# Kernel tuning notes

Hardware: AMD Instinct MI355X
Metric: run time of the kernel (lower is better)

The kernel has to match this reference:

```python
import jax, jax.numpy as jnp
import numpy as np

EMB = 1024
HEADS = 16
HEAD_DIM = EMB // HEADS
B, S = 4, 2048


def setup_inputs() -> dict:
    key = jax.random.key(0)
    ks = jax.random.split(key, 7)
    sc = 1.0 / np.sqrt(EMB)
    return {
        "query": jax.random.normal(ks[0], (B, S, EMB), jnp.float32),
        "key": jax.random.normal(ks[1], (B, S, EMB), jnp.float32),
        "value": jax.random.normal(ks[2], (B, S, EMB), jnp.float32),
        "Wq": jax.random.normal(ks[3], (EMB, EMB), jnp.float32) * sc,
        "Wk": jax.random.normal(ks[4], (EMB, EMB), jnp.float32) * sc,
        "Wv": jax.random.normal(ks[5], (EMB, EMB), jnp.float32) * sc,
        "Wo": jax.random.normal(ks[6], (EMB, EMB), jnp.float32) * sc,
    }


def reference(query, key, value, Wq, Wk, Wv, Wo):
    # nn.Linear applies x @ W^T; W stored as [out, in]
    def split_heads(x):  # [B,S,E] -> [B,H,S,D]
        return x.reshape(B, -1, HEADS, HEAD_DIM).transpose(0, 2, 1, 3)

    q = split_heads(query @ Wq.T)
    k = split_heads(key @ Wk.T)
    v = split_heads(value @ Wv.T)
    scores = jnp.einsum('bhse,bhte->bhst', q, k) / np.sqrt(HEAD_DIM).astype(np.float32)
    attn = jax.nn.softmax(scores, axis=-1)
    ctx = jnp.einsum('bhst,bhtd->bshd', attn, v)  # [B,S,H,D]
    out = ctx.reshape(B, -1, EMB) @ Wo.T
    return out
```

## Files before the change

kernel.cpp:

```cpp
#include <hip/hip_runtime.h>
#include <hip/hip_bf16.h>

#define EMB   1024
#define HEADS 16
#define HDIM  64
#define BB    4
#define SS    2048
#define MROWS (BB*SS)

typedef __bf16 bf16_t;
typedef __bf16 bf16x4_t __attribute__((ext_vector_type(4)));
typedef __bf16 bf16x8   __attribute__((ext_vector_type(8)));
typedef float  f32x4    __attribute__((ext_vector_type(4)));

__device__ __forceinline__ void glds16(const void* g, void* l) {
  __builtin_amdgcn_global_load_lds(
      (const __attribute__((address_space(1))) void*)g,
      (__attribute__((address_space(3))) void*)l, 16, 0, 0);
}

__launch_bounds__(256)
__global__ void cast_multi(const float* s0, const float* s1, const float* s2,
                           const float* s3, const float* s4, const float* s5,
                           const float* s6,
                           bf16_t* d0, bf16_t* d1, bf16_t* d2, bf16_t* d3,
                           bf16_t* d4, bf16_t* d5, bf16_t* d6, int nact) {
  const int z = blockIdx.z;
  if (z >= nact && blockIdx.x >= 512) return;
  const float* ss[7] = {s0, s1, s2, s3, s4, s5, s6};
  bf16_t*      dd[7] = {d0, d1, d2, d3, d4, d5, d6};
  const float* s = ss[z];
  bf16_t*      d = dd[z];
  const int i = (blockIdx.x*256 + threadIdx.x) * 8;
  const f32x4 a = *(const f32x4*)&s[i];
  const f32x4 b = *(const f32x4*)&s[i+4];
  bf16x8 r;
  r[0]=(bf16_t)a[0]; r[1]=(bf16_t)a[1]; r[2]=(bf16_t)a[2]; r[3]=(bf16_t)a[3];
  r[4]=(bf16_t)b[0]; r[5]=(bf16_t)b[1]; r[6]=(bf16_t)b[2]; r[7]=(bf16_t)b[3];
  *(bf16x8*)&d[i] = r;
}

__launch_bounds__(256)
__global__ void cast_f32_bf16(const float* __restrict__ src, bf16_t* __restrict__ dst) {
  const int i = (blockIdx.x*256 + threadIdx.x) * 8;
  const f32x4 a = *(const f32x4*)&src[i];
  const f32x4 b = *(const f32x4*)&src[i+4];
  bf16x8 r;
  r[0]=(bf16_t)a[0]; r[1]=(bf16_t)a[1]; r[2]=(bf16_t)a[2]; r[3]=(bf16_t)a[3];
  r[4]=(bf16_t)b[0]; r[5]=(bf16_t)b[1]; r[6]=(bf16_t)b[2]; r[7]=(bf16_t)b[3];
  *(bf16x8*)&dst[i] = r;
}

__device__ __forceinline__ void gemm_core(const bf16_t* __restrict__ A,
                                          const bf16_t* __restrict__ W,
                                          bf16_t* As, bf16_t* Bs,
                                          f32x4 acc[4][4],
                                          int bm0, int bn0,
                                          int wave, int lane) {
  const int quad = lane >> 4, l16 = lane & 15;
  const int wm = wave >> 1, wn = wave & 1;
  for (int k0 = 0; k0 < EMB; k0 += 32) {
#pragma unroll
    for (int j = 0; j < 2; ++j) {
      const int i   = wave*2 + j;
      const int row = i*16 + (lane >> 2);
      const int col = (lane & 3) * 8;
      glds16(A + (size_t)(bm0 + row)*EMB + k0 + col, &As[i*512]);
      glds16(W + (size_t)(bn0 + row)*EMB + k0 + col, &Bs[i*512]);
    }
    __syncthreads();

    bf16x8 a[4], b[4];
#pragma unroll
    for (int t = 0; t < 4; ++t) {
      a[t] = *(const bf16x8*)&As[(wm*64 + t*16 + l16)*32 + quad*8];
      b[t] = *(const bf16x8*)&Bs[(wn*64 + t*16 + l16)*32 + quad*8];
    }
#pragma unroll
    for (int mt = 0; mt < 4; ++mt)
#pragma unroll
      for (int nt = 0; nt < 4; ++nt)
        acc[mt][nt] = __builtin_amdgcn_mfma_f32_16x16x32_bf16(a[mt], b[nt], acc[mt][nt], 0, 0, 0);
    __syncthreads();
  }
}

__launch_bounds__(256)
__global__ void gemm_qkv(const bf16_t* A0, const bf16_t* A1, const bf16_t* A2,
                         const bf16_t* W0, const bf16_t* W1, const bf16_t* W2,
                         bf16_t* C0, bf16_t* C1, bf16_t* C2,
                         float sscale, int zbase) {
  __shared__ __align__(16) bf16_t As[128*32];
  __shared__ __align__(16) bf16_t Bs[128*32];
  const int tid  = threadIdx.x;
  const int wave = tid >> 6, lane = tid & 63;
  const int quad = lane >> 4, l16 = lane & 15;
  const int wm = wave >> 1, wn = wave & 1;

  const int fid = blockIdx.x + 8*(blockIdx.y + 64*blockIdx.z);
  const int xcd = fid & 7, s = fid >> 3;
  const int bn0 = (s & 7) * 128;
  const int p   = xcd + 8*(s >> 3);
  const int z   = (p >> 6) + zbase;
  const int bm0 = (p & 63) * 128;

  const bf16_t* A = (z == 0) ? A0 : (z == 1) ? A1 : A2;
  const bf16_t* W = (z == 0) ? W0 : (z == 1) ? W1 : W2;
  bf16_t*       C = (z == 0) ? C0 : (z == 1) ? C1 : C2;
  const float oscale = (z == 0) ? sscale : 1.0f;

  f32x4 acc[4][4] = {};
  gemm_core(A, W, As, Bs, acc, bm0, bn0, wave, lane);

  if (z == 2) {
    const int bb = bm0 >> 11;
    const int T  = ((bm0 & 2047) >> 6) + wm;
    const int h  = (bn0 >> 6) + wn;
    bf16_t* base = C + ((size_t)(bb*HEADS + h)*32 + T)*4096;
#pragma unroll
    for (int ks = 0; ks < 2; ++ks)
#pragma unroll
      for (int nt = 0; nt < 4; ++nt) {
        bf16x8 v;
#pragma unroll
        for (int r = 0; r < 4; ++r) {
          v[r]     = (bf16_t)acc[2*ks][nt][r];
          v[4 + r] = (bf16_t)acc[2*ks + 1][nt][r];
        }
        *(bf16x8*)&base[((nt*2 + ks)*64 + quad*16 + l16)*8] = v;
      }
  } else {
#pragma unroll
    for (int mt = 0; mt < 4; ++mt) {
      const int row = bm0 + wm*64 + mt*16 + quad*4;
#pragma unroll
      for (int nt = 0; nt < 4; ++nt) {
        const int col = bn0 + wn*64 + nt*16 + l16;
#pragma unroll
        for (int r = 0; r < 4; ++r)
          C[(size_t)(row + r)*EMB + col] = (bf16_t)(acc[mt][nt][r] * oscale);
      }
    }
  }
}

__launch_bounds__(256)
__global__ void gemm_out(const bf16_t* __restrict__ A, const bf16_t* __restrict__ W,
                         float* __restrict__ C) {
  __shared__ __align__(16) bf16_t As[128*32];
  __shared__ __align__(16) bf16_t Bs[128*32];
  const int tid  = threadIdx.x;
  const int wave = tid >> 6, lane = tid & 63;
  const int quad = lane >> 4, l16 = lane & 15;
  const int wm = wave >> 1, wn = wave & 1;

  const int fid = blockIdx.x + 8*blockIdx.y;
  const int xcd = fid & 7, s = fid >> 3;
  const int bn0 = (s & 7) * 128;
  const int bm0 = (xcd*8 + (s >> 3)) * 128;

  f32x4 acc[4][4] = {};
  gemm_core(A, W, As, Bs, acc, bm0, bn0, wave, lane);

#pragma unroll
  for (int mt = 0; mt < 4; ++mt) {
    const int row = bm0 + wm*64 + mt*16 + quad*4;
#pragma unroll
    for (int nt = 0; nt < 4; ++nt) {
      const int col = bn0 + wn*64 + nt*16 + l16;
#pragma unroll
      for (int r = 0; r < 4; ++r)
        C[(size_t)(row + r)*EMB + col] = acc[mt][nt][r];
    }
  }
}

__launch_bounds__(256)
__global__ void attn(const bf16_t* Qp, const bf16_t* __restrict__ Kp,
                     const bf16_t* __restrict__ Vt, bf16_t* Cx) {
  __shared__ __align__(16) bf16_t Ks[2*64*32];
  __shared__ __align__(16) bf16_t Vs[4096];

  const int tid  = threadIdx.x;
  const int wave = tid >> 6, lane = tid & 63;
  const int quad = lane >> 4, l16 = lane & 15;

  const int fid  = blockIdx.x + 16*(blockIdx.y + 16*blockIdx.z);
  const int xcd  = fid & 7, s = fid >> 3;
  const int q0   = (s & 15) * 128;
  const int pair = xcd*8 + (s >> 4);
  const int h    = pair & 15;
  const int b    = pair >> 4;

  bf16x8 qf[2][2];
#pragma unroll
  for (int mb = 0; mb < 2; ++mb) {
    const size_t qr = (size_t)(b*SS + q0 + wave*32 + mb*16 + l16)*EMB + h*HDIM;
#pragma unroll
    for (int ks = 0; ks < 2; ++ks)
      qf[mb][ks] = *(const bf16x8*)&Qp[qr + ks*32 + quad*8];
  }

  const bf16_t* Kb = Kp + (size_t)b*SS*EMB + h*HDIM;
  const bf16_t* Vb = Vt + ((size_t)(b*HEADS + h)*32)*4096;

  f32x4 o[2][4] = {};
  float lsum[2] = {0.f, 0.f};

  for (int t0 = 0; t0 < SS; t0 += 64) {
#pragma unroll
    for (int c = 0; c < 2; ++c) {
      const int i   = wave + c*4;
      const int r   = (i & 3)*16 + (lane >> 2);
      const int col = (lane & 3)*8;
      glds16(Kb + (size_t)(t0 + r)*EMB + c*32 + col, &Ks[i*512]);
      glds16(Vb + (size_t)(t0 >> 6)*4096 + i*512 + lane*8, &Vs[i*512]);
    }
    __syncthreads();

    f32x4 st[2][4] = {};
#pragma unroll
    for (int cb = 0; cb < 4; ++cb) {
      const bf16x8 kf0 = *(const bf16x8*)&Ks[(cb*16 + l16)*32 + quad*8];
      const bf16x8 kf1 = *(const bf16x8*)&Ks[2048 + (cb*16 + l16)*32 + quad*8];
#pragma unroll
      for (int mb = 0; mb < 2; ++mb) {
        st[mb][cb] = __builtin_amdgcn_mfma_f32_16x16x32_bf16(kf0, qf[mb][0], st[mb][cb], 0, 0, 0);
        st[mb][cb] = __builtin_amdgcn_mfma_f32_16x16x32_bf16(kf1, qf[mb][1], st[mb][cb], 0, 0, 0);
      }
    }

    bf16x8 pb[2][2];
#pragma unroll
    for (int mb = 0; mb < 2; ++mb) {
      float ls = 0.f;
#pragma unroll
      for (int kb = 0; kb < 4; ++kb)
#pragma unroll
        for (int r = 0; r < 4; ++r) {
          const float p = __builtin_amdgcn_exp2f(st[mb][kb][r]);
          st[mb][kb][r] = p;
          ls += p;
        }
      lsum[mb] += ls;
#pragma unroll
      for (int ks = 0; ks < 2; ++ks)
#pragma unroll
        for (int r = 0; r < 4; ++r) {
          pb[mb][ks][r]     = (bf16_t)st[mb][2*ks][r];
          pb[mb][ks][4 + r] = (bf16_t)st[mb][2*ks + 1][r];
        }
    }

#pragma unroll
    for (int ks = 0; ks < 2; ++ks)
#pragma unroll
      for (int dt = 0; dt < 4; ++dt) {
        const bf16x8 vf = *(const bf16x8*)&Vs[((dt*2 + ks)*64 + quad*16 + l16)*8];
#pragma unroll
        for (int mb = 0; mb < 2; ++mb)
          o[mb][dt] = __builtin_amdgcn_mfma_f32_16x16x32_bf16(vf, pb[mb][ks], o[mb][dt], 0, 0, 0);
      }
    __syncthreads();
  }

#pragma unroll
  for (int mb = 0; mb < 2; ++mb) {
    float l = lsum[mb];
    l += __shfl_xor(l, 16, 64);
    l += __shfl_xor(l, 32, 64);
    const float inv = 1.0f / l;
    const size_t row = (size_t)(b*SS + q0 + wave*32 + mb*16 + l16)*EMB + h*HDIM;
#pragma unroll
    for (int dt = 0; dt < 4; ++dt) {
      bf16x4_t v;
#pragma unroll
      for (int r = 0; r < 4; ++r) v[r] = (bf16_t)(o[mb][dt][r] * inv);
      *(bf16x4_t*)&Cx[row + dt*16 + quad*4] = v;
    }
  }
}

extern "C" void kernel_launch(void* const* d_in, const int* in_sizes, int n_in,
                              void* d_out, int out_size, void* d_ws, size_t ws_size,
                              hipStream_t stream) {
  (void)in_sizes; (void)n_in; (void)out_size;
  const float* query = (const float*)d_in[0];
  const float* key   = (const float*)d_in[1];
  const float* value = (const float*)d_in[2];
  const float* WqF   = (const float*)d_in[3];
  const float* WkF   = (const float*)d_in[4];
  const float* WvF   = (const float*)d_in[5];
  const float* WoF   = (const float*)d_in[6];

  const size_t AN = (size_t)MROWS*EMB;
  const size_t WN = (size_t)EMB*EMB;
  float* out = (float*)d_out;
  bf16_t* S5 = (bf16_t*)d_out;
  bf16_t* S6 = S5 + AN;

  const float sscale = 0.125f * 1.44269504f;

  const dim3 gqkv(EMB/128, MROWS/128, 3);
  const dim3 gqk (EMB/128, MROWS/128, 2);
  const dim3 gv  (EMB/128, MROWS/128, 1);
  const dim3 gg  (EMB/128, MROWS/128);
  const dim3 gattn(SS/128, HEADS, BB);

  if (ws_size >= (size_t)(4*AN + 4*WN) * sizeof(bf16_t)) {
    bf16_t* qb  = (bf16_t*)d_ws;
    bf16_t* kb  = qb + AN;
    bf16_t* vb  = kb + AN;
    bf16_t* S2  = vb + AN;
    bf16_t* Wqb = S2 + AN;
    bf16_t* Wkb = Wqb + WN;
    bf16_t* Wvb = Wkb + WN;
    bf16_t* Wob = Wvb + WN;

    cast_multi<<<dim3(AN/2048, 1, 7), 256, 0, stream>>>(
        query, key, value, WqF, WkF, WvF, WoF,
        qb, kb, vb, Wqb, Wkb, Wvb, Wob, 3);
    gemm_qkv<<<gqkv, 256, 0, stream>>>(qb, kb, vb, Wqb, Wkb, Wvb,
                                       S2, S6, S5, sscale, 0);
    attn<<<gattn, 256, 0, stream>>>(S2, S6, S5, S2);
    gemm_out<<<gg, 256, 0, stream>>>(S2, Wob, out);
  } else {
    bf16_t* S1  = (bf16_t*)d_ws;
    bf16_t* S2  = S1 + AN;
    bf16_t* Wqb = S2 + AN;
    bf16_t* Wkb = Wqb + WN;
    bf16_t* Wvb = Wkb + WN;
    bf16_t* Wob = Wvb + WN;

    cast_multi<<<dim3(AN/2048, 1, 6), 256, 0, stream>>>(
        query, key, WqF, WkF, WvF, WoF, WoF,
        S1, S5, Wqb, Wkb, Wvb, Wob, Wob, 2);
    gemm_qkv<<<gqk, 256, 0, stream>>>(S1, S5, S1, Wqb, Wkb, Wvb,
                                      S2, S6, S5, sscale, 0);
    cast_f32_bf16<<<dim3(AN/2048), 256, 0, stream>>>(value, S1);
    gemm_qkv<<<gv, 256, 0, stream>>>(S1, S1, S1, Wvb, Wvb, Wvb,
                                     S5, S5, S5, 1.0f, 2);
    attn<<<gattn, 256, 0, stream>>>(S2, S6, S5, S2);
    gemm_out<<<gg, 256, 0, stream>>>(S2, Wob, out);
  }
}
```

Measured before the change: 323.8 us.

## Double-buffer K/V tiles in attention and deepen GEMM K-step to 64

The attention kernel now double-buffers K and V tiles in LDS, issuing async global-to-LDS loads for the next tile before computing on the current one, so load latency can overlap with MFMA work. The shared GEMM core processes 64 columns of K per iteration instead of 32, halving the number of barriers and enlarging the A/B LDS tiles. Both changes raise LDS usage per block, which may lower occupancy.

```diff
diff --git a/kernel.cpp b/kernel.cpp
--- a/kernel.cpp
+++ b/kernel.cpp
@@ -59,28 +59,33 @@
                                           int wave, int lane) {
   const int quad = lane >> 4, l16 = lane & 15;
   const int wm = wave >> 1, wn = wave & 1;
-  for (int k0 = 0; k0 < EMB; k0 += 32) {
-#pragma unroll
-    for (int j = 0; j < 2; ++j) {
-      const int i   = wave*2 + j;
-      const int row = i*16 + (lane >> 2);
-      const int col = (lane & 3) * 8;
-      glds16(A + (size_t)(bm0 + row)*EMB + k0 + col, &As[i*512]);
-      glds16(W + (size_t)(bn0 + row)*EMB + k0 + col, &Bs[i*512]);
-    }
+  for (int k0 = 0; k0 < EMB; k0 += 64) {
+#pragma unroll
+    for (int ks = 0; ks < 2; ++ks)
+#pragma unroll
+      for (int c = 0; c < 2; ++c) {
+        const int j   = wave*2 + c;
+        const int row = j*16 + (lane >> 2);
+        const int col = ks*32 + (lane & 3)*8;
+        glds16(A + (size_t)(bm0 + row)*EMB + k0 + col, &As[ks*4096 + j*512]);
+        glds16(W + (size_t)(bn0 + row)*EMB + k0 + col, &Bs[ks*4096 + j*512]);
+      }
     __syncthreads();
 
-    bf16x8 a[4], b[4];
-#pragma unroll
-    for (int t = 0; t < 4; ++t) {
-      a[t] = *(const bf16x8*)&As[(wm*64 + t*16 + l16)*32 + quad*8];
-      b[t] = *(const bf16x8*)&Bs[(wn*64 + t*16 + l16)*32 + quad*8];
-    }
-#pragma unroll
-    for (int mt = 0; mt < 4; ++mt)
-#pragma unroll
-      for (int nt = 0; nt < 4; ++nt)
-        acc[mt][nt] = __builtin_amdgcn_mfma_f32_16x16x32_bf16(a[mt], b[nt], acc[mt][nt], 0, 0, 0);
+#pragma unroll
+    for (int ks = 0; ks < 2; ++ks) {
+      bf16x8 a[4], b[4];
+#pragma unroll
+      for (int t = 0; t < 4; ++t) {
+        a[t] = *(const bf16x8*)&As[ks*4096 + (wm*64 + t*16 + l16)*32 + quad*8];
+        b[t] = *(const bf16x8*)&Bs[ks*4096 + (wn*64 + t*16 + l16)*32 + quad*8];
+      }
+#pragma unroll
+      for (int mt = 0; mt < 4; ++mt)
+#pragma unroll
+        for (int nt = 0; nt < 4; ++nt)
+          acc[mt][nt] = __builtin_amdgcn_mfma_f32_16x16x32_bf16(a[mt], b[nt], acc[mt][nt], 0, 0, 0);
+    }
     __syncthreads();
   }
 }
@@ -90,8 +95,8 @@
                          const bf16_t* W0, const bf16_t* W1, const bf16_t* W2,
                          bf16_t* C0, bf16_t* C1, bf16_t* C2,
                          float sscale, int zbase) {
-  __shared__ __align__(16) bf16_t As[128*32];
-  __shared__ __align__(16) bf16_t Bs[128*32];
+  __shared__ __align__(16) bf16_t As[128*64];
+  __shared__ __align__(16) bf16_t Bs[128*64];
   const int tid  = threadIdx.x;
   const int wave = tid >> 6, lane = tid & 63;
   const int quad = lane >> 4, l16 = lane & 15;
@@ -147,8 +152,8 @@
 __launch_bounds__(256)
 __global__ void gemm_out(const bf16_t* __restrict__ A, const bf16_t* __restrict__ W,
                          float* __restrict__ C) {
-  __shared__ __align__(16) bf16_t As[128*32];
-  __shared__ __align__(16) bf16_t Bs[128*32];
+  __shared__ __align__(16) bf16_t As[128*64];
+  __shared__ __align__(16) bf16_t Bs[128*64];
   const int tid  = threadIdx.x;
   const int wave = tid >> 6, lane = tid & 63;
   const int quad = lane >> 4, l16 = lane & 15;
@@ -178,8 +183,8 @@
 __launch_bounds__(256)
 __global__ void attn(const bf16_t* Qp, const bf16_t* __restrict__ Kp,
                      const bf16_t* __restrict__ Vt, bf16_t* Cx) {
-  __shared__ __align__(16) bf16_t Ks[2*64*32];
-  __shared__ __align__(16) bf16_t Vs[4096];
+  __shared__ __align__(16) bf16_t Ks[2][4096];
+  __shared__ __align__(16) bf16_t Vs[2][4096];
 
   const int tid  = threadIdx.x;
   const int wave = tid >> 6, lane = tid & 63;
@@ -207,29 +212,31 @@
   f32x4 o[2][4] = {};
   float lsum[2] = {0.f, 0.f};
 
-  for (int t0 = 0; t0 < SS; t0 += 64) {
+  auto stage = [&](int buf, int t0) {
 #pragma unroll
     for (int c = 0; c < 2; ++c) {
       const int i   = wave + c*4;
       const int r   = (i & 3)*16 + (lane >> 2);
       const int col = (lane & 3)*8;
-      glds16(Kb + (size_t)(t0 + r)*EMB + c*32 + col, &Ks[i*512]);
-      glds16(Vb + (size_t)(t0 >> 6)*4096 + i*512 + lane*8, &Vs[i*512]);
-    }
-    __syncthreads();
-
+      glds16(Kb + (size_t)(t0 + r)*EMB + c*32 + col, &Ks[buf][i*512]);
+      glds16(Vb + (size_t)(t0 >> 6)*4096 + i*512 + lane*8, &Vs[buf][i*512]);
+    }
+  };
+
+  auto compute = [&](int buf) {
+    const bf16_t* Kss = Ks[buf];
+    const bf16_t* Vss = Vs[buf];
     f32x4 st[2][4] = {};
 #pragma unroll
     for (int cb = 0; cb < 4; ++cb) {
-      const bf16x8 kf0 = *(const bf16x8*)&Ks[(cb*16 + l16)*32 + quad*8];
-      const bf16x8 kf1 = *(const bf16x8*)&Ks[2048 + (cb*16 + l16)*32 + quad*8];
+      const bf16x8 kf0 = *(const bf16x8*)&Kss[(cb*16 + l16)*32 + quad*8];
+      const bf16x8 kf1 = *(const bf16x8*)&Kss[2048 + (cb*16 + l16)*32 + quad*8];
 #pragma unroll
       for (int mb = 0; mb < 2; ++mb) {
         st[mb][cb] = __builtin_amdgcn_mfma_f32_16x16x32_bf16(kf0, qf[mb][0], st[mb][cb], 0, 0, 0);
         st[mb][cb] = __builtin_amdgcn_mfma_f32_16x16x32_bf16(kf1, qf[mb][1], st[mb][cb], 0, 0, 0);
       }
     }
-
     bf16x8 pb[2][2];
 #pragma unroll
     for (int mb = 0; mb < 2; ++mb) {
@@ -251,17 +258,25 @@
           pb[mb][ks][4 + r] = (bf16_t)st[mb][2*ks + 1][r];
         }
     }
-
 #pragma unroll
     for (int ks = 0; ks < 2; ++ks)
 #pragma unroll
       for (int dt = 0; dt < 4; ++dt) {
-        const bf16x8 vf = *(const bf16x8*)&Vs[((dt*2 + ks)*64 + quad*16 + l16)*8];
+        const bf16x8 vf = *(const bf16x8*)&Vss[((dt*2 + ks)*64 + quad*16 + l16)*8];
 #pragma unroll
         for (int mb = 0; mb < 2; ++mb)
           o[mb][dt] = __builtin_amdgcn_mfma_f32_16x16x32_bf16(vf, pb[mb][ks], o[mb][dt], 0, 0, 0);
       }
+  };
+
+  stage(0, 0);
+  for (int t = 0; t < SS/64; t += 2) {
     __syncthreads();
+    if (t + 1 < SS/64) stage(1, (t+1)*64);
+    compute(0);
+    __syncthreads();
+    if (t + 2 < SS/64) stage(0, (t+2)*64);
+    compute(1);
   }
 
 #pragma unroll
```

Result: no change. 329.3 us (+1.7%).

## Load GEMM and attention operands directly from global memory, bypassing LDS staging

Applied to the files above, without the earlier changes.

Removes the shared-memory staging (global_load_lds plus barriers) from the GEMM core and the attention kernel, so each wave loads its MFMA fragments straight from global memory into registers. This drops the LDS traffic and the __syncthreads barriers. In exchange, data that several waves shared through LDS is now fetched redundantly from global memory or cache (A/W tiles twice per block, K/V four times per block), and the strided per-lane accesses may coalesce worse.

```diff
diff --git a/kernel.cpp b/kernel.cpp
--- a/kernel.cpp
+++ b/kernel.cpp
@@ -12,12 +12,6 @@
 typedef __bf16 bf16x4_t __attribute__((ext_vector_type(4)));
 typedef __bf16 bf16x8   __attribute__((ext_vector_type(8)));
 typedef float  f32x4    __attribute__((ext_vector_type(4)));
-
-__device__ __forceinline__ void glds16(const void* g, void* l) {
-  __builtin_amdgcn_global_load_lds(
-      (const __attribute__((address_space(1))) void*)g,
-      (__attribute__((address_space(3))) void*)l, 16, 0, 0);
-}
 
 __launch_bounds__(256)
 __global__ void cast_multi(const float* s0, const float* s1, const float* s2,
@@ -53,35 +47,26 @@
 
 __device__ __forceinline__ void gemm_core(const bf16_t* __restrict__ A,
                                           const bf16_t* __restrict__ W,
-                                          bf16_t* As, bf16_t* Bs,
                                           f32x4 acc[4][4],
                                           int bm0, int bn0,
                                           int wave, int lane) {
   const int quad = lane >> 4, l16 = lane & 15;
   const int wm = wave >> 1, wn = wave & 1;
+  const bf16_t* Ab = A + (size_t)(bm0 + wm*64 + l16)*EMB + quad*8;
+  const bf16_t* Wb = W + (size_t)(bn0 + wn*64 + l16)*EMB + quad*8;
+#pragma unroll 2
   for (int k0 = 0; k0 < EMB; k0 += 32) {
-#pragma unroll
-    for (int j = 0; j < 2; ++j) {
-      const int i   = wave*2 + j;
-      const int row = i*16 + (lane >> 2);
-      const int col = (lane & 3) * 8;
-      glds16(A + (size_t)(bm0 + row)*EMB + k0 + col, &As[i*512]);
-      glds16(W + (size_t)(bn0 + row)*EMB + k0 + col, &Bs[i*512]);
-    }
-    __syncthreads();
-
     bf16x8 a[4], b[4];
 #pragma unroll
     for (int t = 0; t < 4; ++t) {
-      a[t] = *(const bf16x8*)&As[(wm*64 + t*16 + l16)*32 + quad*8];
-      b[t] = *(const bf16x8*)&Bs[(wn*64 + t*16 + l16)*32 + quad*8];
+      a[t] = *(const bf16x8*)&Ab[(size_t)t*16*EMB + k0];
+      b[t] = *(const bf16x8*)&Wb[(size_t)t*16*EMB + k0];
     }
 #pragma unroll
     for (int mt = 0; mt < 4; ++mt)
 #pragma unroll
       for (int nt = 0; nt < 4; ++nt)
         acc[mt][nt] = __builtin_amdgcn_mfma_f32_16x16x32_bf16(a[mt], b[nt], acc[mt][nt], 0, 0, 0);
-    __syncthreads();
   }
 }
 
@@ -90,8 +75,6 @@
                          const bf16_t* W0, const bf16_t* W1, const bf16_t* W2,
                          bf16_t* C0, bf16_t* C1, bf16_t* C2,
                          float sscale, int zbase) {
-  __shared__ __align__(16) bf16_t As[128*32];
-  __shared__ __align__(16) bf16_t Bs[128*32];
   const int tid  = threadIdx.x;
   const int wave = tid >> 6, lane = tid & 63;
   const int quad = lane >> 4, l16 = lane & 15;
@@ -110,7 +93,7 @@
   const float oscale = (z == 0) ? sscale : 1.0f;
 
   f32x4 acc[4][4] = {};
-  gemm_core(A, W, As, Bs, acc, bm0, bn0, wave, lane);
+  gemm_core(A, W, acc, bm0, bn0, wave, lane);
 
   if (z == 2) {
     const int bb = bm0 >> 11;
@@ -147,8 +130,6 @@
 __launch_bounds__(256)
 __global__ void gemm_out(const bf16_t* __restrict__ A, const bf16_t* __restrict__ W,
                          float* __restrict__ C) {
-  __shared__ __align__(16) bf16_t As[128*32];
-  __shared__ __align__(16) bf16_t Bs[128*32];
   const int tid  = threadIdx.x;
   const int wave = tid >> 6, lane = tid & 63;
   const int quad = lane >> 4, l16 = lane & 15;
@@ -160,7 +141,7 @@
   const int bm0 = (xcd*8 + (s >> 3)) * 128;
 
   f32x4 acc[4][4] = {};
-  gemm_core(A, W, As, Bs, acc, bm0, bn0, wave, lane);
+  gemm_core(A, W, acc, bm0, bn0, wave, lane);
 
 #pragma unroll
   for (int mt = 0; mt < 4; ++mt) {
@@ -178,9 +159,6 @@
 __launch_bounds__(256)
 __global__ void attn(const bf16_t* Qp, const bf16_t* __restrict__ Kp,
                      const bf16_t* __restrict__ Vt, bf16_t* Cx) {
-  __shared__ __align__(16) bf16_t Ks[2*64*32];
-  __shared__ __align__(16) bf16_t Vs[4096];
-
   const int tid  = threadIdx.x;
   const int wave = tid >> 6, lane = tid & 63;
   const int quad = lane >> 4, l16 = lane & 15;
@@ -201,28 +179,19 @@
       qf[mb][ks] = *(const bf16x8*)&Qp[qr + ks*32 + quad*8];
   }
 
-  const bf16_t* Kb = Kp + (size_t)b*SS*EMB + h*HDIM;
-  const bf16_t* Vb = Vt + ((size_t)(b*HEADS + h)*32)*4096;
+  const bf16_t* Kb = Kp + (size_t)b*SS*EMB + h*HDIM + quad*8;
+  const bf16_t* Vb = Vt + ((size_t)(b*HEADS + h)*32)*4096 + lane*8;
 
   f32x4 o[2][4] = {};
   float lsum[2] = {0.f, 0.f};
 
   for (int t0 = 0; t0 < SS; t0 += 64) {
-#pragma unroll
-    for (int c = 0; c < 2; ++c) {
-      const int i   = wave + c*4;
-      const int r   = (i & 3)*16 + (lane >> 2);
-      const int col = (lane & 3)*8;
-      glds16(Kb + (size_t)(t0 + r)*EMB + c*32 + col, &Ks[i*512]);
-      glds16(Vb + (size_t)(t0 >> 6)*4096 + i*512 + lane*8, &Vs[i*512]);
-    }
-    __syncthreads();
-
     f32x4 st[2][4] = {};
 #pragma unroll
     for (int cb = 0; cb < 4; ++cb) {
-      const bf16x8 kf0 = *(const bf16x8*)&Ks[(cb*16 + l16)*32 + quad*8];
-      const bf16x8 kf1 = *(const bf16x8*)&Ks[2048 + (cb*16 + l16)*32 + quad*8];
+      const bf16_t* kr = Kb + (size_t)(t0 + cb*16 + l16)*EMB;
+      const bf16x8 kf0 = *(const bf16x8*)&kr[0];
+      const bf16x8 kf1 = *(const bf16x8*)&kr[32];
 #pragma unroll
       for (int mb = 0; mb < 2; ++mb) {
         st[mb][cb] = __builtin_amdgcn_mfma_f32_16x16x32_bf16(kf0, qf[mb][0], st[mb][cb], 0, 0, 0);
@@ -252,16 +221,16 @@
         }
     }
 
+    const bf16_t* vr = Vb + (size_t)(t0 >> 6)*4096;
 #pragma unroll
     for (int ks = 0; ks < 2; ++ks)
 #pragma unroll
       for (int dt = 0; dt < 4; ++dt) {
-        const bf16x8 vf = *(const bf16x8*)&Vs[((dt*2 + ks)*64 + quad*16 + l16)*8];
+        const bf16x8 vf = *(const bf16x8*)&vr[(dt*2 + ks)*512];
 #pragma unroll
         for (int mb = 0; mb < 2; ++mb)
           o[mb][dt] = __builtin_amdgcn_mfma_f32_16x16x32_bf16(vf, pb[mb][ks], o[mb][dt], 0, 0, 0);
       }
-    __syncthreads();
   }
 
 #pragma unroll
```

Measured after the change: 587.5 us. +81.4%, slower.
